# Performance work log

Measured on AMD Instinct MI355X. Metric: run time of the kernel, lower is better.

## Reference

```python
import jax, jax.numpy as jnp
import numpy as np
from jax import lax

WIN = 7
K1, K2 = 0.01, 0.03
NP_ = WIN * WIN
COV_NORM = NP_ / (NP_ - 1)


def _box_filter(t, w):
    # t: [B, C, H, W] -> valid 7x7 box mean, [B, C, H-6, W-6]
    B, C, H, W = t.shape
    o = lax.conv_general_dilated(
        t.reshape(B * C, 1, H, W), w, window_strides=(1, 1), padding='VALID',
        dimension_numbers=('NCHW', 'OIHW', 'NCHW'))
    return o.reshape(B, C, H - WIN + 1, W - WIN + 1)


def setup_inputs() -> dict:
    key = jax.random.key(0)
    kx, ky = jax.random.split(key)
    X = jax.random.uniform(kx, (32, 3, 512, 512), dtype=jnp.float32)
    Y = jax.random.uniform(ky, (32, 3, 512, 512), dtype=jnp.float32)
    return {"X": X, "Y": Y}


def reference(X, Y):
    data_range = 1.0
    C1 = (K1 * data_range) ** 2
    C2 = (K2 * data_range) ** 2
    w = jnp.full((1, 1, WIN, WIN), 1.0 / NP_, dtype=X.dtype)

    ux = _box_filter(X, w)
    uy = _box_filter(Y, w)
    uxx = _box_filter(X * X, w)
    uyy = _box_filter(Y * Y, w)
    uxy = _box_filter(X * Y, w)

    vx = COV_NORM * (uxx - ux * ux)
    vy = COV_NORM * (uyy - uy * uy)
    vxy = COV_NORM * (uxy - ux * uy)

    A1 = 2 * ux * uy + C1
    A2 = 2 * vxy + C2
    B1 = ux * ux + uy * uy + C1
    B2 = vx + vy + C2
    S = (A1 * A2) / (B1 * B2)
    # reduced=True: per-channel means then mean over channels == global mean
    # (all channels have identical spatial size)
    return 1.0 - jnp.mean(S)
```

## Files before the change

### kernel.cpp

```cpp
#include <hip/hip_runtime.h>


#define IW    512
#define OUTW  506
#define RBAND 11
#define NB    46
#define NIMG  96
#define NWAVE (NIMG * NB)
#define C1N2  0.2401f
#define C2N2  2.1609f
#define KA    (49.0f/24.0f)
#define KB    (49.0f/48.0f)
#define TOTAL_OUT 24579456.0f

__global__ void ssim_zero(float* acc) {
    if (threadIdx.x == 0) acc[0] = 0.0f;
}

__device__ __forceinline__ float ssim_raw(float Sx, float Sy, float Sxx,
                                          float Syy, float Sxy) {
    float sxsy = Sx * Sy;
    float p    = fmaf(Sx, Sx, Sy * Sy);
    float a1   = fmaf(2.0f, sxsy, C1N2);
    float b1   = p + C1N2;
    float a2   = fmaf(KA, fmaf(49.0f, Sxy, -sxsy), C2N2);
    float b2   = fmaf(KB, fmaf(49.0f, Sxx + Syy, -p), C2N2);
    return (a1 * a2) * __builtin_amdgcn_rcpf(b1 * b2);
}

__device__ __forceinline__ void acc_add(float cs[5][8],
                                        const float4& xa, const float4& xb,
                                        const float4& ya, const float4& yb) {
    float xs[8] = {xa.x, xa.y, xa.z, xa.w, xb.x, xb.y, xb.z, xb.w};
    float ys[8] = {ya.x, ya.y, ya.z, ya.w, yb.x, yb.y, yb.z, yb.w};
#pragma unroll
    for (int c = 0; c < 8; ++c) {
        cs[0][c] += xs[c];
        cs[1][c] += ys[c];
        cs[2][c] = fmaf(xs[c], xs[c], cs[2][c]);
        cs[3][c] = fmaf(ys[c], ys[c], cs[3][c]);
        cs[4][c] = fmaf(xs[c], ys[c], cs[4][c]);
    }
}

__device__ __forceinline__ void acc_sub(float cs[5][8],
                                        const float4& xa, const float4& xb,
                                        const float4& ya, const float4& yb) {
    float xs[8] = {xa.x, xa.y, xa.z, xa.w, xb.x, xb.y, xb.z, xb.w};
    float ys[8] = {ya.x, ya.y, ya.z, ya.w, yb.x, yb.y, yb.z, yb.w};
#pragma unroll
    for (int c = 0; c < 8; ++c) {
        cs[0][c] -= xs[c];
        cs[1][c] -= ys[c];
        cs[2][c] = fmaf(-xs[c], xs[c], cs[2][c]);
        cs[3][c] = fmaf(-ys[c], ys[c], cs[3][c]);
        cs[4][c] = fmaf(-xs[c], ys[c], cs[4][c]);
    }
}

__global__ __launch_bounds__(256) void ssim_main(const float* __restrict__ X,
                                                 const float* __restrict__ Y,
                                                 float* __restrict__ acc) {
    const int t  = threadIdx.x;
    const int s  = t & 63;
    const int w  = blockIdx.x * 4 + (t >> 6);
    const int img  = w / NB;
    const int band = w % NB;
    const int r0 = band * RBAND;

    const float4* X4 = (const float4*)(X + (size_t)img * IW * IW);
    const float4* Y4 = (const float4*)(Y + (size_t)img * IW * IW);
    const int ci = 2 * s;

    float cs[5][8];
#pragma unroll
    for (int q = 0; q < 5; ++q)
#pragma unroll
        for (int c = 0; c < 8; ++c) cs[q][c] = 0.0f;

#pragma unroll
    for (int i = 0; i < 6; ++i) {
        const int r = r0 + i;
        float4 xa = X4[r * 128 + ci], xb = X4[r * 128 + ci + 1];
        float4 ya = Y4[r * 128 + ci], yb = Y4[r * 128 + ci + 1];
        acc_add(cs, xa, xb, ya, yb);
    }

    float4 nxa = X4[(r0 + 6) * 128 + ci], nxb = X4[(r0 + 6) * 128 + ci + 1];
    float4 nya = Y4[(r0 + 6) * 128 + ci], nyb = Y4[(r0 + 6) * 128 + ci + 1];
    float4 rxa = X4[r0 * 128 + ci],       rxb = X4[r0 * 128 + ci + 1];
    float4 rya = Y4[r0 * 128 + ci],       ryb = Y4[r0 * 128 + ci + 1];

    float accS = 0.0f;

    for (int j = 0; j < RBAND; ++j) {
        acc_add(cs, nxa, nxb, nya, nyb);

        {
            const int rn = min(r0 + j + 7, IW - 1);
            nxa = X4[rn * 128 + ci]; nxb = X4[rn * 128 + ci + 1];
            nya = Y4[rn * 128 + ci]; nyb = Y4[rn * 128 + ci + 1];
        }

        float halo[5][6];
#pragma unroll
        for (int q = 0; q < 5; ++q)
#pragma unroll
            for (int k = 0; k < 6; ++k)
                halo[q][k] = __shfl_down(cs[q][k], 1, 64);

        float W[5];
#pragma unroll
        for (int q = 0; q < 5; ++q)
            W[q] = ((cs[q][0] + cs[q][1]) + (cs[q][2] + cs[q][3])) +
                   ((cs[q][4] + cs[q][5]) + cs[q][6]);
        accS += ssim_raw(W[0], W[1], W[2], W[3], W[4]);
#pragma unroll
        for (int m = 1; m < 8; ++m) {
#pragma unroll
            for (int q = 0; q < 5; ++q) {
                float cn = (m == 1) ? cs[q][7] : halo[q][m - 2];
                W[q] += cn - cs[q][m - 1];
            }
            float Sv = ssim_raw(W[0], W[1], W[2], W[3], W[4]);
            if (m < 2) accS += Sv;
            else       accS += (8 * s + m < OUTW) ? Sv : 0.0f;
        }

        acc_sub(cs, rxa, rxb, rya, ryb);
        {
            const int rr = r0 + j + 1;
            rxa = X4[rr * 128 + ci]; rxb = X4[rr * 128 + ci + 1];
            rya = Y4[rr * 128 + ci]; ryb = Y4[rr * 128 + ci + 1];
        }
    }

#pragma unroll
    for (int off = 32; off > 0; off >>= 1)
        accS += __shfl_down(accS, off, 64);
    if (s == 0) atomicAdd(acc, accS);
}

__global__ void ssim_finalize(const float* __restrict__ acc,
                              float* __restrict__ out) {
    if (threadIdx.x == 0) out[0] = 1.0f - acc[0] / TOTAL_OUT;
}

extern "C" void kernel_launch(void* const* d_in, const int* in_sizes, int n_in,
                              void* d_out, int out_size, void* d_ws, size_t ws_size,
                              hipStream_t stream) {
    const float* X = (const float*)d_in[0];
    const float* Y = (const float*)d_in[1];
    float* accum = (float*)d_ws;
    float* out = (float*)d_out;

    hipLaunchKernelGGL(ssim_zero, dim3(1), dim3(64), 0, stream, accum);
    hipLaunchKernelGGL(ssim_main, dim3(NWAVE / 4), dim3(256), 0, stream,
                       X, Y, accum);
    hipLaunchKernelGGL(ssim_finalize, dim3(1), dim3(64), 0, stream, accum, out);
}
```

Before: 265.7 us.

## Share column sums through LDS across block and use per-block partials

Each 256-thread block now covers a full image row width, with each thread holding a float2 column pair. Column running sums go to a double-row shared-memory plane, and half the block computes horizontal windows for each of two rows per iteration. This replaces the wave-shuffle halo exchange with an LDS exchange and doubles the band height to 22 rows, which reduces halo reloads. The global atomic and zero kernel give way to per-block partials reduced in a finalize kernel, at the cost of two __syncthreads per pair of rows.

```diff
diff --git a/kernel.cpp b/kernel.cpp
--- a/kernel.cpp
+++ b/kernel.cpp
@@ -3,19 +3,15 @@
 
 #define IW    512
 #define OUTW  506
-#define RBAND 11
-#define NB    46
+#define BAND  22
+#define NBANDS 23
 #define NIMG  96
-#define NWAVE (NIMG * NB)
+#define NPART (NBANDS * NIMG)
 #define C1N2  0.2401f
 #define C2N2  2.1609f
 #define KA    (49.0f/24.0f)
 #define KB    (49.0f/48.0f)
 #define TOTAL_OUT 24579456.0f
-
-__global__ void ssim_zero(float* acc) {
-    if (threadIdx.x == 0) acc[0] = 0.0f;
-}
 
 __device__ __forceinline__ float ssim_raw(float Sx, float Sy, float Sxx,
                                           float Syy, float Sxy) {
@@ -28,122 +24,136 @@
     return (a1 * a2) * __builtin_amdgcn_rcpf(b1 * b2);
 }
 
-__device__ __forceinline__ void acc_add(float cs[5][8],
-                                        const float4& xa, const float4& xb,
-                                        const float4& ya, const float4& yb) {
-    float xs[8] = {xa.x, xa.y, xa.z, xa.w, xb.x, xb.y, xb.z, xb.w};
-    float ys[8] = {ya.x, ya.y, ya.z, ya.w, yb.x, yb.y, yb.z, yb.w};
-#pragma unroll
-    for (int c = 0; c < 8; ++c) {
-        cs[0][c] += xs[c];
-        cs[1][c] += ys[c];
-        cs[2][c] = fmaf(xs[c], xs[c], cs[2][c]);
-        cs[3][c] = fmaf(ys[c], ys[c], cs[3][c]);
-        cs[4][c] = fmaf(xs[c], ys[c], cs[4][c]);
-    }
-}
+__global__ __launch_bounds__(256, 5) void ssim_main(const float* __restrict__ X,
+                                                    const float* __restrict__ Y,
+                                                    float* __restrict__ partials) {
+    __shared__ float plane[2][5][65 * 12];
+    __shared__ float wsum[4];
 
-__device__ __forceinline__ void acc_sub(float cs[5][8],
-                                        const float4& xa, const float4& xb,
-                                        const float4& ya, const float4& yb) {
-    float xs[8] = {xa.x, xa.y, xa.z, xa.w, xb.x, xb.y, xb.z, xb.w};
-    float ys[8] = {ya.x, ya.y, ya.z, ya.w, yb.x, yb.y, yb.z, yb.w};
-#pragma unroll
-    for (int c = 0; c < 8; ++c) {
-        cs[0][c] -= xs[c];
-        cs[1][c] -= ys[c];
-        cs[2][c] = fmaf(-xs[c], xs[c], cs[2][c]);
-        cs[3][c] = fmaf(-ys[c], ys[c], cs[3][c]);
-        cs[4][c] = fmaf(-xs[c], ys[c], cs[4][c]);
-    }
-}
+    const int t    = threadIdx.x;
+    const int band = blockIdx.x;
+    const int img  = blockIdx.y;
+    const int r0   = band * BAND;
+    const float2* X2 = (const float2*)(X + (size_t)img * IW * IW);
+    const float2* Y2 = (const float2*)(Y + (size_t)img * IW * IW);
 
-__global__ __launch_bounds__(256) void ssim_main(const float* __restrict__ X,
-                                                 const float* __restrict__ Y,
-                                                 float* __restrict__ acc) {
-    const int t  = threadIdx.x;
-    const int s  = t & 63;
-    const int w  = blockIdx.x * 4 + (t >> 6);
-    const int img  = w / NB;
-    const int band = w % NB;
-    const int r0 = band * RBAND;
-
-    const float4* X4 = (const float4*)(X + (size_t)img * IW * IW);
-    const float4* Y4 = (const float4*)(Y + (size_t)img * IW * IW);
-    const int ci = 2 * s;
-
-    float cs[5][8];
-#pragma unroll
-    for (int q = 0; q < 5; ++q)
-#pragma unroll
-        for (int c = 0; c < 8; ++c) cs[q][c] = 0.0f;
+    float sxa=0,sxb=0, sya=0,syb=0, sxxa=0,sxxb=0, syya=0,syyb=0, sxya=0,sxyb=0;
 
 #pragma unroll
     for (int i = 0; i < 6; ++i) {
-        const int r = r0 + i;
-        float4 xa = X4[r * 128 + ci], xb = X4[r * 128 + ci + 1];
-        float4 ya = Y4[r * 128 + ci], yb = Y4[r * 128 + ci + 1];
-        acc_add(cs, xa, xb, ya, yb);
+        float2 x = X2[(r0 + i) * 256 + t];
+        float2 y = Y2[(r0 + i) * 256 + t];
+        sxa += x.x;  sxb += x.y;  sya += y.x;  syb += y.y;
+        sxxa = fmaf(x.x,x.x,sxxa); sxxb = fmaf(x.y,x.y,sxxb);
+        syya = fmaf(y.x,y.x,syya); syyb = fmaf(y.y,y.y,syyb);
+        sxya = fmaf(x.x,y.x,sxya); sxyb = fmaf(x.y,y.y,sxyb);
     }
 
-    float4 nxa = X4[(r0 + 6) * 128 + ci], nxb = X4[(r0 + 6) * 128 + ci + 1];
-    float4 nya = Y4[(r0 + 6) * 128 + ci], nyb = Y4[(r0 + 6) * 128 + ci + 1];
-    float4 rxa = X4[r0 * 128 + ci],       rxb = X4[r0 * 128 + ci + 1];
-    float4 rya = Y4[r0 * 128 + ci],       ryb = Y4[r0 * 128 + ci + 1];
+    const int woff = 12 * (t >> 2) + 2 * (t & 3);
+
+    const int hw  = t >> 7;
+    const int ht  = t & 127;
+    const int p0  = 4 * ht;
+    const int u   = ht >> 1;
+    const int off = (ht & 1) * 4;
+    const int aA = 12 * u + off;
+    const int aB = 12 * u + (off ? 12 : 4);
+    const int aC = 12 * u + 12 + off;
+
+    float2 nx[2], ny[2], rx[2], ry[2];
+#pragma unroll
+    for (int k = 0; k < 2; ++k) {
+        nx[k] = X2[(r0 + 6 + k) * 256 + t];
+        ny[k] = Y2[(r0 + 6 + k) * 256 + t];
+        rx[k] = X2[(r0 + k) * 256 + t];
+        ry[k] = Y2[(r0 + k) * 256 + t];
+    }
 
     float accS = 0.0f;
 
-    for (int j = 0; j < RBAND; ++j) {
-        acc_add(cs, nxa, nxb, nya, nyb);
+    for (int j = 0; j < BAND; j += 2) {
+#pragma unroll
+        for (int k = 0; k < 2; ++k) {
+            float2 x = nx[k], y = ny[k];
+            sxa += x.x;  sxb += x.y;  sya += y.x;  syb += y.y;
+            sxxa = fmaf(x.x,x.x,sxxa); sxxb = fmaf(x.y,x.y,sxxb);
+            syya = fmaf(y.x,y.x,syya); syyb = fmaf(y.y,y.y,syyb);
+            sxya = fmaf(x.x,y.x,sxya); sxyb = fmaf(x.y,y.y,sxyb);
+            *(float2*)&plane[k][0][woff] = make_float2(sxa,  sxb);
+            *(float2*)&plane[k][1][woff] = make_float2(sya,  syb);
+            *(float2*)&plane[k][2][woff] = make_float2(sxxa, sxxb);
+            *(float2*)&plane[k][3][woff] = make_float2(syya, syyb);
+            *(float2*)&plane[k][4][woff] = make_float2(sxya, sxyb);
+            float2 ox = rx[k], oy = ry[k];
+            sxa -= ox.x;  sxb -= ox.y;  sya -= oy.x;  syb -= oy.y;
+            sxxa = fmaf(-ox.x,ox.x,sxxa); sxxb = fmaf(-ox.y,ox.y,sxxb);
+            syya = fmaf(-oy.x,oy.x,syya); syyb = fmaf(-oy.y,oy.y,syyb);
+            sxya = fmaf(-ox.x,oy.x,sxya); sxyb = fmaf(-ox.y,oy.y,sxyb);
+        }
+        if (j + 2 < BAND) {
+#pragma unroll
+            for (int k = 0; k < 2; ++k) {
+                nx[k] = X2[(r0 + j + 8 + k) * 256 + t];
+                ny[k] = Y2[(r0 + j + 8 + k) * 256 + t];
+                rx[k] = X2[(r0 + j + 2 + k) * 256 + t];
+                ry[k] = Y2[(r0 + j + 2 + k) * 256 + t];
+            }
+        }
+        __syncthreads();
 
         {
-            const int rn = min(r0 + j + 7, IW - 1);
-            nxa = X4[rn * 128 + ci]; nxb = X4[rn * 128 + ci + 1];
-            nya = Y4[rn * 128 + ci]; nyb = Y4[rn * 128 + ci + 1];
-        }
-
-        float halo[5][6];
-#pragma unroll
-        for (int q = 0; q < 5; ++q)
-#pragma unroll
-            for (int k = 0; k < 6; ++k)
-                halo[q][k] = __shfl_down(cs[q][k], 1, 64);
-
-        float W[5];
-#pragma unroll
-        for (int q = 0; q < 5; ++q)
-            W[q] = ((cs[q][0] + cs[q][1]) + (cs[q][2] + cs[q][3])) +
-                   ((cs[q][4] + cs[q][5]) + cs[q][6]);
-        accS += ssim_raw(W[0], W[1], W[2], W[3], W[4]);
-#pragma unroll
-        for (int m = 1; m < 8; ++m) {
+            float c[5][10];
 #pragma unroll
             for (int q = 0; q < 5; ++q) {
-                float cn = (m == 1) ? cs[q][7] : halo[q][m - 2];
-                W[q] += cn - cs[q][m - 1];
+                const float* pl = plane[hw][q];
+                float4 A = *(const float4*)(pl + aA);
+                float4 B = *(const float4*)(pl + aB);
+                float2 C = *(const float2*)(pl + aC);
+                c[q][0]=A.x; c[q][1]=A.y; c[q][2]=A.z; c[q][3]=A.w;
+                c[q][4]=B.x; c[q][5]=B.y; c[q][6]=B.z; c[q][7]=B.w;
+                c[q][8]=C.x; c[q][9]=C.y;
             }
-            float Sv = ssim_raw(W[0], W[1], W[2], W[3], W[4]);
-            if (m < 2) accS += Sv;
-            else       accS += (8 * s + m < OUTW) ? Sv : 0.0f;
+            float W[5];
+#pragma unroll
+            for (int q = 0; q < 5; ++q)
+                W[q] = ((c[q][0] + c[q][1]) + (c[q][2] + c[q][3])) +
+                       ((c[q][4] + c[q][5]) + c[q][6]);
+            accS += (p0 < OUTW) ? ssim_raw(W[0],W[1],W[2],W[3],W[4]) : 0.0f;
+#pragma unroll
+            for (int m = 1; m < 4; ++m) {
+#pragma unroll
+                for (int q = 0; q < 5; ++q)
+                    W[q] += c[q][m + 6] - c[q][m - 1];
+                float Sv = ssim_raw(W[0],W[1],W[2],W[3],W[4]);
+                accS += (p0 + m < OUTW) ? Sv : 0.0f;
+            }
         }
-
-        acc_sub(cs, rxa, rxb, rya, ryb);
-        {
-            const int rr = r0 + j + 1;
-            rxa = X4[rr * 128 + ci]; rxb = X4[rr * 128 + ci + 1];
-            rya = Y4[rr * 128 + ci]; ryb = Y4[rr * 128 + ci + 1];
-        }
+        __syncthreads();
     }
 
 #pragma unroll
-    for (int off = 32; off > 0; off >>= 1)
-        accS += __shfl_down(accS, off, 64);
-    if (s == 0) atomicAdd(acc, accS);
+    for (int o = 32; o > 0; o >>= 1)
+        accS += __shfl_down(accS, o, 64);
+    if ((t & 63) == 0) wsum[t >> 6] = accS;
+    __syncthreads();
+    if (t == 0)
+        partials[blockIdx.y * NBANDS + blockIdx.x] =
+            (wsum[0] + wsum[1]) + (wsum[2] + wsum[3]);
 }
 
-__global__ void ssim_finalize(const float* __restrict__ acc,
-                              float* __restrict__ out) {
-    if (threadIdx.x == 0) out[0] = 1.0f - acc[0] / TOTAL_OUT;
+__global__ __launch_bounds__(256) void ssim_finalize(const float* __restrict__ partials,
+                                                     float* __restrict__ out) {
+    __shared__ float wsum[4];
+    const int t = threadIdx.x;
+    float v = 0.0f;
+    for (int i = t; i < NPART; i += 256) v += partials[i];
+#pragma unroll
+    for (int o = 32; o > 0; o >>= 1)
+        v += __shfl_down(v, o, 64);
+    if ((t & 63) == 0) wsum[t >> 6] = v;
+    __syncthreads();
+    if (t == 0)
+        out[0] = 1.0f - ((wsum[0] + wsum[1]) + (wsum[2] + wsum[3])) / TOTAL_OUT;
 }
 
 extern "C" void kernel_launch(void* const* d_in, const int* in_sizes, int n_in,
@@ -151,11 +161,11 @@
                               hipStream_t stream) {
     const float* X = (const float*)d_in[0];
     const float* Y = (const float*)d_in[1];
-    float* accum = (float*)d_ws;
+    float* partials = (float*)d_ws;
     float* out = (float*)d_out;
 
-    hipLaunchKernelGGL(ssim_zero, dim3(1), dim3(64), 0, stream, accum);
-    hipLaunchKernelGGL(ssim_main, dim3(NWAVE / 4), dim3(256), 0, stream,
-                       X, Y, accum);
-    hipLaunchKernelGGL(ssim_finalize, dim3(1), dim3(64), 0, stream, accum, out);
+    hipLaunchKernelGGL(ssim_main, dim3(NBANDS, NIMG), dim3(256), 0, stream,
+                       X, Y, partials);
+    hipLaunchKernelGGL(ssim_finalize, dim3(1), dim3(256), 0, stream,
+                       partials, out);
 }
```

Measured after the change: 230.1 us. -13.4%, faster.
